# Optimization experiments

Hardware: AMD Instinct MI355X
Metric: run time of the kernel (lower is better)

Reference implementation:

```python
import jax, jax.numpy as jnp
import numpy as np

U = 8192       # num users
N = 100000     # num items
H = 50         # history length per user
E = U * H      # total edges
QD = 128       # query_dim
D = 256        # in_dim
WSCALE = 0.01  # small weight init to keep exp() in fp32 range


def setup_inputs() -> dict:
    key = jax.random.key(0)
    ks = jax.random.split(key, 10)
    user_queries = jax.random.normal(ks[0], (U, QD), dtype=jnp.float32)
    item_features = jax.random.normal(ks[1], (N, D), dtype=jnp.float32)
    # flattened user_history_map: every user has exactly H history items
    batch_user_indices = jnp.repeat(jnp.arange(U, dtype=jnp.int64), H)
    batch_item_indices = jax.random.randint(ks[2], (E,), 0, N, dtype=jnp.int64)
    Wq = jax.random.normal(ks[3], (QD, D), dtype=jnp.float32) * WSCALE
    bq = jnp.zeros((D,), dtype=jnp.float32)
    Wk = jax.random.normal(ks[4], (D, D), dtype=jnp.float32) * WSCALE
    bk = jnp.zeros((D,), dtype=jnp.float32)
    Wv = jax.random.normal(ks[5], (D, D), dtype=jnp.float32) * WSCALE
    bv = jnp.zeros((D,), dtype=jnp.float32)
    return {
        'user_queries': user_queries, 'item_features': item_features,
        'Wq': Wq, 'bq': bq, 'Wk': Wk, 'bk': bk, 'Wv': Wv, 'bv': bv,
        'batch_user_indices': batch_user_indices,
        'batch_item_indices': batch_item_indices,
    }


def reference(user_queries, item_features, Wq, bq, Wk, bk, Wv, bv,
              batch_user_indices, batch_item_indices):
    num_users = user_queries.shape[0]
    projected_queries = user_queries @ Wq + bq            # [U, D]
    feats = item_features[batch_item_indices]             # [E, D] gather
    keys = feats @ Wk + bk                                # [E, D]
    values = feats @ Wv + bv                              # [E, D]
    queries_expanded = projected_queries[batch_user_indices]  # [E, D]
    attn_scores = jnp.sum(queries_expanded * keys, axis=1)    # [E]
    # NOTE: original code computes 'max_scores' with scatter_add_, which is a
    # per-user SUM, not a max. Reproduced faithfully.
    max_scores = jax.ops.segment_sum(attn_scores, batch_user_indices,
                                     num_segments=num_users)   # [U]
    exp_scores = jnp.exp(attn_scores - max_scores[batch_user_indices])
    sum_exp = jax.ops.segment_sum(exp_scores, batch_user_indices,
                                  num_segments=num_users)      # [U]
    attn_weights = exp_scores / (sum_exp[batch_user_indices] + 1e-12)
    user_profiles = jax.ops.segment_sum(values * attn_weights[:, None],
                                        batch_user_indices,
                                        num_segments=num_users)  # [U, D]
    return user_profiles
```

## Files before the change

### kernel.cpp

```cpp
#include <hip/hip_runtime.h>
#include <math.h>

#define U 8192
#define NITEMS 100000
#define H 50
#define QD 128
#define D 256
#define BMG 8
#define NRMAX 13

__device__ __forceinline__ float wave_bcast_sum64(float x) {
    float t = x;
    int y;
    y = __builtin_amdgcn_update_dpp(0, __float_as_int(t), 0xB1, 0xF, 0xF, true);
    t += __int_as_float(y);
    y = __builtin_amdgcn_update_dpp(0, __float_as_int(t), 0x4E, 0xF, 0xF, true);
    t += __int_as_float(y);
    y = __builtin_amdgcn_update_dpp(0, __float_as_int(t), 0x124, 0xF, 0xF, true);
    t += __int_as_float(y);
    y = __builtin_amdgcn_update_dpp(0, __float_as_int(t), 0x128, 0xF, 0xF, true);
    t += __int_as_float(y);
    y = __builtin_amdgcn_update_dpp(0, __float_as_int(t), 0x142, 0xA, 0xF, true);
    t += __int_as_float(y);
    y = __builtin_amdgcn_update_dpp(0, __float_as_int(t), 0x143, 0xC, 0xF, true);
    t += __int_as_float(y);
    return __int_as_float(__builtin_amdgcn_readlane(__float_as_int(t), 63));
}

__device__ __forceinline__ float block_reduce_256(float v, float* sred) {
    #pragma unroll
    for (int off = 32; off >= 1; off >>= 1)
        v += __shfl_xor(v, off, 64);
    int wave = threadIdx.x >> 6;
    int lane = threadIdx.x & 63;
    if (lane == 0) sred[wave] = v;
    __syncthreads();
    float s;
    if (threadIdx.x == 0) {
        s = sred[0] + sred[1] + sred[2] + sred[3];
        sred[0] = s;
    }
    __syncthreads();
    s = sred[0];
    __syncthreads();
    return s;
}

__global__ void __launch_bounds__(256) upa_precompute(
    const float* __restrict__ Wq, const float* __restrict__ bq,
    const float* __restrict__ Wk, const float* __restrict__ bk,
    float* __restrict__ M, float* __restrict__ bqt,
    float* __restrict__ wb, float* __restrict__ c0) {
    __shared__ float row[D];
    __shared__ float sred[4];
    int k = blockIdx.x;
    int t = threadIdx.x;
    if (k < QD) {
        row[t] = (t < D) ? Wq[k * D + t] : 0.f;
        __syncthreads();
        const float4* wkr = (const float4*)(Wk + (size_t)t * D);
        const float4* rr  = (const float4*)row;
        float acc = 0.f;
        #pragma unroll 4
        for (int i = 0; i < D / 4; ++i) {
            float4 a = rr[i]; float4 b = wkr[i];
            acc += a.x * b.x + a.y * b.y + a.z * b.z + a.w * b.w;
        }
        M[k * D + t] = acc;
        float p = row[t] * bk[t];
        float s = block_reduce_256(p, sred);
        if (t == 0) wb[k] = s;
    } else {
        row[t] = bq[t];
        __syncthreads();
        const float4* wkr = (const float4*)(Wk + (size_t)t * D);
        const float4* rr  = (const float4*)row;
        float acc = 0.f;
        #pragma unroll 4
        for (int i = 0; i < D / 4; ++i) {
            float4 a = rr[i]; float4 b = wkr[i];
            acc += a.x * b.x + a.y * b.y + a.z * b.z + a.w * b.w;
        }
        bqt[t] = acc;
        float p = row[t] * bk[t];
        float s = block_reduce_256(p, sred);
        if (t == 0) c0[0] = s;
    }
}

__global__ void __launch_bounds__(256) upa_qt(
    const float* __restrict__ uq, const float* __restrict__ M,
    const float* __restrict__ bqt, float* __restrict__ qt) {
    __shared__ float A[BMG][QD];
    int u0 = blockIdx.x * BMG;
    int t = threadIdx.x;
    const float4* src = (const float4*)(uq + (size_t)u0 * QD);
    float4* dst = (float4*)&A[0][0];
    for (int i = t; i < BMG * QD / 4; i += 256) dst[i] = src[i];
    __syncthreads();
    float acc[BMG];
    #pragma unroll
    for (int r = 0; r < BMG; ++r) acc[r] = 0.f;
    for (int k8 = 0; k8 < QD; k8 += 8) {
        float m[8];
        #pragma unroll
        for (int i = 0; i < 8; ++i) m[i] = M[(size_t)(k8 + i) * D + t];
        #pragma unroll
        for (int r = 0; r < BMG; ++r) {
            float4 a0 = *((const float4*)&A[r][k8]);
            float4 a1 = *((const float4*)&A[r][k8 + 4]);
            acc[r] += a0.x * m[0] + a0.y * m[1] + a0.z * m[2] + a0.w * m[3]
                    + a1.x * m[4] + a1.y * m[5] + a1.z * m[6] + a1.w * m[7];
        }
    }
    float bb = bqt[t];
    #pragma unroll
    for (int r = 0; r < BMG; ++r) qt[(size_t)(u0 + r) * D + t] = acc[r] + bb;
}

__global__ void __launch_bounds__(256, 5) upa_attn(
    const float* __restrict__ qt, const float* __restrict__ uq,
    const float* __restrict__ wb, const float* __restrict__ c0,
    const float* __restrict__ feats, const int* __restrict__ item_idx,
    float* __restrict__ agg, float* __restrict__ sw) {
    __shared__ float pagg[4][D];
    __shared__ float pE[4], pS[4];
    int u = blockIdx.x;
    int t = threadIdx.x;
    int wave = t >> 6, lane = t & 63;

    float p = uq[(size_t)u * QD + lane] * wb[lane]
            + uq[(size_t)u * QD + 64 + lane] * wb[64 + lane];
    float qb = wave_bcast_sum64(p) + c0[0];

    float4 q = ((const float4*)(qt + (size_t)u * D))[lane];

    int ll = lane < H ? lane : H - 1;
    int idxv = item_idx[(size_t)u * H + ll];

    float4 acc = make_float4(0.f, 0.f, 0.f, 0.f);
    float E = 0.f, S = 0.f;
    #pragma unroll
    for (int r = 0; r < NRMAX; ++r) {
        int j = 4 * r + wave;
        if (j < H) {
            int sidx = __builtin_amdgcn_readlane(idxv, j);
            float4 v = ((const float4*)(feats + (size_t)sidx * D))[lane];
            float part = v.x * q.x + v.y * q.y + v.z * q.z + v.w * q.w;
            float s = wave_bcast_sum64(part) + qb;
            float e = __expf(s);
            S += s;
            E += e;
            acc.x += e * v.x;
            acc.y += e * v.y;
            acc.z += e * v.z;
            acc.w += e * v.w;
        }
    }

    ((float4*)pagg[wave])[lane] = acc;
    if (lane == 0) { pE[wave] = E; pS[wave] = S; }
    __syncthreads();
    float Et = pE[0] + pE[1] + pE[2] + pE[3];
    float St = pS[0] + pS[1] + pS[2] + pS[3];
    float inv = 1.f / (Et + 1e-12f * __expf(St));
    agg[(size_t)u * D + t] =
        (pagg[0][t] + pagg[1][t] + pagg[2][t] + pagg[3][t]) * inv;
    if (t == 0) sw[u] = Et * inv;
}

__global__ void __launch_bounds__(256) upa_out(
    const float* __restrict__ agg, const float* __restrict__ Wv,
    const float* __restrict__ bv, const float* __restrict__ sw,
    float* __restrict__ out) {
    __shared__ float A[BMG][D];
    int u0 = blockIdx.x * BMG;
    int t = threadIdx.x;
    const float4* src = (const float4*)(agg + (size_t)u0 * D);
    float4* dst = (float4*)&A[0][0];
    for (int i = t; i < BMG * D / 4; i += 256) dst[i] = src[i];
    __syncthreads();
    float acc[BMG];
    #pragma unroll
    for (int r = 0; r < BMG; ++r) acc[r] = 0.f;
    for (int k8 = 0; k8 < D; k8 += 8) {
        float m[8];
        #pragma unroll
        for (int i = 0; i < 8; ++i) m[i] = Wv[(size_t)(k8 + i) * D + t];
        #pragma unroll
        for (int r = 0; r < BMG; ++r) {
            float4 a0 = *((const float4*)&A[r][k8]);
            float4 a1 = *((const float4*)&A[r][k8 + 4]);
            acc[r] += a0.x * m[0] + a0.y * m[1] + a0.z * m[2] + a0.w * m[3]
                    + a1.x * m[4] + a1.y * m[5] + a1.z * m[6] + a1.w * m[7];
        }
    }
    float b = bv[t];
    #pragma unroll
    for (int r = 0; r < BMG; ++r)
        out[(size_t)(u0 + r) * D + t] = acc[r] + b * sw[u0 + r];
}

extern "C" void kernel_launch(void* const* d_in, const int* in_sizes, int n_in,
                              void* d_out, int out_size, void* d_ws, size_t ws_size,
                              hipStream_t stream) {
    const float* uq    = (const float*)d_in[0];
    const float* feats = (const float*)d_in[1];
    const float* Wq    = (const float*)d_in[2];
    const float* bq    = (const float*)d_in[3];
    const float* Wk    = (const float*)d_in[4];
    const float* bk    = (const float*)d_in[5];
    const float* Wv    = (const float*)d_in[6];
    const float* bv    = (const float*)d_in[7];
    const int* item_idx = (const int*)d_in[9];
    float* out = (float*)d_out;

    float* ws  = (float*)d_ws;
    float* M   = ws;
    float* bqt = M + QD * D;
    float* wb  = bqt + D;
    float* c0  = wb + QD;
    float* qt  = c0 + 4;
    float* agg = qt + (size_t)U * D;
    float* sw  = agg + (size_t)U * D;

    upa_precompute<<<QD + 1, 256, 0, stream>>>(Wq, bq, Wk, bk, M, bqt, wb, c0);
    upa_qt<<<U / BMG, 256, 0, stream>>>(uq, M, bqt, qt);
    upa_attn<<<U, 256, 0, stream>>>(qt, uq, wb, c0, feats, item_idx, agg, sw);
    upa_out<<<U / BMG, 256, 0, stream>>>(agg, Wv, bv, sw, out);
}
```

Measured before the change: 122.5 us.

## Fuse query projection, attention, and value projection into one kernel per 8 users

Replaces the three kernels (qt, attn, out) with one fused kernel. Each block handles 8 users, keeps the projected queries and the aggregated vectors in shared memory, and each wave processes two users across all 50 history items. This removes the global round trips for qt, agg and sw and two kernel launches, and gives each wave two independent gather streams to overlap. The cost is only 1024 blocks instead of 8192 for the gather phase, a lower occupancy bound, and a longer serial loop per wave, which may reduce how well memory latency is hidden.

```diff
diff --git a/kernel.cpp b/kernel.cpp
--- a/kernel.cpp
+++ b/kernel.cpp
@@ -7,7 +7,6 @@
 #define QD 128
 #define D 256
 #define BMG 8
-#define NRMAX 13
 
 __device__ __forceinline__ float wave_bcast_sum64(float x) {
     float t = x;
@@ -88,117 +87,114 @@
     }
 }
 
-__global__ void __launch_bounds__(256) upa_qt(
+__global__ void __launch_bounds__(256, 4) upa_fused(
     const float* __restrict__ uq, const float* __restrict__ M,
-    const float* __restrict__ bqt, float* __restrict__ qt) {
+    const float* __restrict__ bqt, const float* __restrict__ wb,
+    const float* __restrict__ c0, const float* __restrict__ feats,
+    const int* __restrict__ item_idx, const float* __restrict__ Wv,
+    const float* __restrict__ bv, float* __restrict__ out) {
     __shared__ float A[BMG][QD];
+    __shared__ float qt_s[BMG][D];
+    __shared__ float agg_s[BMG][D];
+    __shared__ float sw_s[BMG];
     int u0 = blockIdx.x * BMG;
     int t = threadIdx.x;
-    const float4* src = (const float4*)(uq + (size_t)u0 * QD);
-    float4* dst = (float4*)&A[0][0];
-    for (int i = t; i < BMG * QD / 4; i += 256) dst[i] = src[i];
-    __syncthreads();
-    float acc[BMG];
-    #pragma unroll
-    for (int r = 0; r < BMG; ++r) acc[r] = 0.f;
-    for (int k8 = 0; k8 < QD; k8 += 8) {
-        float m[8];
-        #pragma unroll
-        for (int i = 0; i < 8; ++i) m[i] = M[(size_t)(k8 + i) * D + t];
-        #pragma unroll
-        for (int r = 0; r < BMG; ++r) {
-            float4 a0 = *((const float4*)&A[r][k8]);
-            float4 a1 = *((const float4*)&A[r][k8 + 4]);
-            acc[r] += a0.x * m[0] + a0.y * m[1] + a0.z * m[2] + a0.w * m[3]
-                    + a1.x * m[4] + a1.y * m[5] + a1.z * m[6] + a1.w * m[7];
-        }
-    }
-    float bb = bqt[t];
-    #pragma unroll
-    for (int r = 0; r < BMG; ++r) qt[(size_t)(u0 + r) * D + t] = acc[r] + bb;
-}
-
-__global__ void __launch_bounds__(256, 5) upa_attn(
-    const float* __restrict__ qt, const float* __restrict__ uq,
-    const float* __restrict__ wb, const float* __restrict__ c0,
-    const float* __restrict__ feats, const int* __restrict__ item_idx,
-    float* __restrict__ agg, float* __restrict__ sw) {
-    __shared__ float pagg[4][D];
-    __shared__ float pE[4], pS[4];
-    int u = blockIdx.x;
-    int t = threadIdx.x;
     int wave = t >> 6, lane = t & 63;
-
-    float p = uq[(size_t)u * QD + lane] * wb[lane]
-            + uq[(size_t)u * QD + 64 + lane] * wb[64 + lane];
-    float qb = wave_bcast_sum64(p) + c0[0];
-
-    float4 q = ((const float4*)(qt + (size_t)u * D))[lane];
+    int uwA = 2 * wave, uwB = 2 * wave + 1;
 
     int ll = lane < H ? lane : H - 1;
-    int idxv = item_idx[(size_t)u * H + ll];
-
-    float4 acc = make_float4(0.f, 0.f, 0.f, 0.f);
-    float E = 0.f, S = 0.f;
-    #pragma unroll
-    for (int r = 0; r < NRMAX; ++r) {
-        int j = 4 * r + wave;
-        if (j < H) {
-            int sidx = __builtin_amdgcn_readlane(idxv, j);
-            float4 v = ((const float4*)(feats + (size_t)sidx * D))[lane];
-            float part = v.x * q.x + v.y * q.y + v.z * q.z + v.w * q.w;
-            float s = wave_bcast_sum64(part) + qb;
-            float e = __expf(s);
-            S += s;
-            E += e;
-            acc.x += e * v.x;
-            acc.y += e * v.y;
-            acc.z += e * v.z;
-            acc.w += e * v.w;
-        }
-    }
-
-    ((float4*)pagg[wave])[lane] = acc;
-    if (lane == 0) { pE[wave] = E; pS[wave] = S; }
-    __syncthreads();
-    float Et = pE[0] + pE[1] + pE[2] + pE[3];
-    float St = pS[0] + pS[1] + pS[2] + pS[3];
-    float inv = 1.f / (Et + 1e-12f * __expf(St));
-    agg[(size_t)u * D + t] =
-        (pagg[0][t] + pagg[1][t] + pagg[2][t] + pagg[3][t]) * inv;
-    if (t == 0) sw[u] = Et * inv;
-}
-
-__global__ void __launch_bounds__(256) upa_out(
-    const float* __restrict__ agg, const float* __restrict__ Wv,
-    const float* __restrict__ bv, const float* __restrict__ sw,
-    float* __restrict__ out) {
-    __shared__ float A[BMG][D];
-    int u0 = blockIdx.x * BMG;
-    int t = threadIdx.x;
-    const float4* src = (const float4*)(agg + (size_t)u0 * D);
-    float4* dst = (float4*)&A[0][0];
-    for (int i = t; i < BMG * D / 4; i += 256) dst[i] = src[i];
-    __syncthreads();
-    float acc[BMG];
-    #pragma unroll
-    for (int r = 0; r < BMG; ++r) acc[r] = 0.f;
-    for (int k8 = 0; k8 < D; k8 += 8) {
-        float m[8];
-        #pragma unroll
-        for (int i = 0; i < 8; ++i) m[i] = Wv[(size_t)(k8 + i) * D + t];
-        #pragma unroll
-        for (int r = 0; r < BMG; ++r) {
-            float4 a0 = *((const float4*)&A[r][k8]);
-            float4 a1 = *((const float4*)&A[r][k8 + 4]);
-            acc[r] += a0.x * m[0] + a0.y * m[1] + a0.z * m[2] + a0.w * m[3]
-                    + a1.x * m[4] + a1.y * m[5] + a1.z * m[6] + a1.w * m[7];
-        }
-    }
-    float b = bv[t];
-    #pragma unroll
-    for (int r = 0; r < BMG; ++r)
-        out[(size_t)(u0 + r) * D + t] = acc[r] + b * sw[u0 + r];
+    int idxA = item_idx[(size_t)(u0 + uwA) * H + ll];
+    int idxB = item_idx[(size_t)(u0 + uwB) * H + ll];
+
+    {
+        const float4* src = (const float4*)(uq + (size_t)u0 * QD);
+        float4* dst = (float4*)&A[0][0];
+        for (int i = t; i < BMG * QD / 4; i += 256) dst[i] = src[i];
+    }
+    __syncthreads();
+
+    {
+        float acc[BMG];
+        #pragma unroll
+        for (int r = 0; r < BMG; ++r) acc[r] = 0.f;
+        for (int k8 = 0; k8 < QD; k8 += 8) {
+            float m[8];
+            #pragma unroll
+            for (int i = 0; i < 8; ++i) m[i] = M[(size_t)(k8 + i) * D + t];
+            #pragma unroll
+            for (int r = 0; r < BMG; ++r) {
+                float4 a0 = *((const float4*)&A[r][k8]);
+                float4 a1 = *((const float4*)&A[r][k8 + 4]);
+                acc[r] += a0.x * m[0] + a0.y * m[1] + a0.z * m[2] + a0.w * m[3]
+                        + a1.x * m[4] + a1.y * m[5] + a1.z * m[6] + a1.w * m[7];
+            }
+        }
+        float bb = bqt[t];
+        #pragma unroll
+        for (int r = 0; r < BMG; ++r) qt_s[r][t] = acc[r] + bb;
+    }
+
+    float pA = A[uwA][lane] * wb[lane] + A[uwA][64 + lane] * wb[64 + lane];
+    float qbA = wave_bcast_sum64(pA) + c0[0];
+    float pB = A[uwB][lane] * wb[lane] + A[uwB][64 + lane] * wb[64 + lane];
+    float qbB = wave_bcast_sum64(pB) + c0[0];
+    __syncthreads();
+
+    float4 qA = ((const float4*)qt_s[uwA])[lane];
+    float4 qB = ((const float4*)qt_s[uwB])[lane];
+
+    float4 accA = make_float4(0.f, 0.f, 0.f, 0.f);
+    float4 accB = make_float4(0.f, 0.f, 0.f, 0.f);
+    float EA = 0.f, SA = 0.f, EB = 0.f, SB = 0.f;
+    #pragma unroll 2
+    for (int j = 0; j < H; ++j) {
+        int sA = __builtin_amdgcn_readlane(idxA, j);
+        int sB = __builtin_amdgcn_readlane(idxB, j);
+        float4 vA = ((const float4*)(feats + (size_t)sA * D))[lane];
+        float4 vB = ((const float4*)(feats + (size_t)sB * D))[lane];
+        float dA = vA.x * qA.x + vA.y * qA.y + vA.z * qA.z + vA.w * qA.w;
+        float dB = vB.x * qB.x + vB.y * qB.y + vB.z * qB.z + vB.w * qB.w;
+        float sfA = wave_bcast_sum64(dA) + qbA;
+        float sfB = wave_bcast_sum64(dB) + qbB;
+        float eA = __expf(sfA);
+        float eB = __expf(sfB);
+        SA += sfA; EA += eA;
+        SB += sfB; EB += eB;
+        accA.x += eA * vA.x; accA.y += eA * vA.y;
+        accA.z += eA * vA.z; accA.w += eA * vA.w;
+        accB.x += eB * vB.x; accB.y += eB * vB.y;
+        accB.z += eB * vB.z; accB.w += eB * vB.w;
+    }
+    float invA = 1.f / (EA + 1e-12f * __expf(SA));
+    float invB = 1.f / (EB + 1e-12f * __expf(SB));
+    ((float4*)agg_s[uwA])[lane] =
+        make_float4(accA.x * invA, accA.y * invA, accA.z * invA, accA.w * invA);
+    ((float4*)agg_s[uwB])[lane] =
+        make_float4(accB.x * invB, accB.y * invB, accB.z * invB, accB.w * invB);
+    if (lane == 0) { sw_s[uwA] = EA * invA; sw_s[uwB] = EB * invB; }
+    __syncthreads();
+
+    {
+        float acc[BMG];
+        #pragma unroll
+        for (int r = 0; r < BMG; ++r) acc[r] = 0.f;
+        for (int k8 = 0; k8 < D; k8 += 8) {
+            float m[8];
+            #pragma unroll
+            for (int i = 0; i < 8; ++i) m[i] = Wv[(size_t)(k8 + i) * D + t];
+            #pragma unroll
+            for (int r = 0; r < BMG; ++r) {
+                float4 a0 = *((const float4*)&agg_s[r][k8]);
+                float4 a1 = *((const float4*)&agg_s[r][k8 + 4]);
+                acc[r] += a0.x * m[0] + a0.y * m[1] + a0.z * m[2] + a0.w * m[3]
+                        + a1.x * m[4] + a1.y * m[5] + a1.z * m[6] + a1.w * m[7];
+            }
+        }
+        float b = bv[t];
+        #pragma unroll
+        for (int r = 0; r < BMG; ++r)
+            out[(size_t)(u0 + r) * D + t] = acc[r] + b * sw_s[r];
+    }
 }
 
 extern "C" void kernel_launch(void* const* d_in, const int* in_sizes, int n_in,
@@ -220,12 +216,8 @@
     float* bqt = M + QD * D;
     float* wb  = bqt + D;
     float* c0  = wb + QD;
-    float* qt  = c0 + 4;
-    float* agg = qt + (size_t)U * D;
-    float* sw  = agg + (size_t)U * D;
 
     upa_precompute<<<QD + 1, 256, 0, stream>>>(Wq, bq, Wk, bk, M, bqt, wb, c0);
-    upa_qt<<<U / BMG, 256, 0, stream>>>(uq, M, bqt, qt);
-    upa_attn<<<U, 256, 0, stream>>>(qt, uq, wb, c0, feats, item_idx, agg, sw);
-    upa_out<<<U / BMG, 256, 0, stream>>>(agg, Wv, bv, sw, out);
-}
+    upa_fused<<<U / BMG, 256, 0, stream>>>(uq, M, bqt, wb, c0, feats, item_idx,
+                                           Wv, bv, out);
+}
```

Measured after the change: 105.9 us (median of 2 runs). 1.16x faster.
